# Performance work log

Hardware: AMD Instinct MI355X
Metric: run time of the kernel (lower is better)

## Reference

```python
import jax, jax.numpy as jnp
import numpy as np

N = 30000      # particles
E = 300000     # directed edges
H = 128        # hidden size
L = 10         # GNN layers
EMB = 16       # particle-type embedding size
T = 5          # velocity history window
NTYPES = 9
RADIUS = 0.05
OUT = 2
NODE_IN = 2 * T + 4 + EMB  # 30


def _mlp_ln(x, W1, b1, W2, b2, W3, b3, g, be):
    # Linear-ReLU-Linear-ReLU-Linear-LayerNorm (matches node/edge encoders and GraphNet blocks)
    h = jax.nn.relu(x @ W1 + b1)
    h = jax.nn.relu(h @ W2 + b2)
    h = h @ W3 + b3
    mu = jnp.mean(h, axis=-1, keepdims=True)
    var = jnp.mean((h - mu) ** 2, axis=-1, keepdims=True)
    return (h - mu) * jax.lax.rsqrt(var + 1e-5) * g + be


def setup_inputs() -> dict:
    key = jax.random.key(0)
    ks = iter(jax.random.split(key, 48))
    nx = lambda: next(ks)
    inp = {}
    inp["vel"] = jax.random.normal(nx(), (N, T, 2), jnp.float32) * 0.01
    inp["pos"] = jax.random.uniform(nx(), (N, 2), dtype=jnp.float32)
    inp["bounds"] = jnp.array([[0.0, 1.0], [0.0, 1.0]], jnp.float32)  # [dim, (lo,hi)]
    inp["tgt_pos"] = jax.random.uniform(nx(), (N, 2), dtype=jnp.float32)
    inp["particle_type"] = jax.random.randint(nx(), (N,), 0, NTYPES, jnp.int32)
    inp["nonk_mask"] = jax.random.randint(nx(), (N,), 0, 2, jnp.int32)
    inp["senders"] = jax.random.randint(nx(), (E,), 0, N, jnp.int32)
    inp["receivers"] = jax.random.randint(nx(), (E,), 0, N, jnp.int32)
    inp["emb"] = jax.random.normal(nx(), (NTYPES, EMB), jnp.float32) * 0.1

    def mlp_p(pre, din, lead=()):
        w = lambda i, o: jax.random.normal(nx(), lead + (i, o), jnp.float32) / np.sqrt(i)
        inp[pre + "_W1"] = w(din, H); inp[pre + "_b1"] = jnp.zeros(lead + (H,), jnp.float32)
        inp[pre + "_W2"] = w(H, H);   inp[pre + "_b2"] = jnp.zeros(lead + (H,), jnp.float32)
        inp[pre + "_W3"] = w(H, H);   inp[pre + "_b3"] = jnp.zeros(lead + (H,), jnp.float32)
        inp[pre + "_g"] = jnp.ones(lead + (H,), jnp.float32)
        inp[pre + "_be"] = jnp.zeros(lead + (H,), jnp.float32)

    mlp_p("ne", NODE_IN)          # node encoder
    mlp_p("ee", 3)                # edge encoder
    mlp_p("ge", 3 * H, (L,))      # per-layer edge-update MLPs
    mlp_p("gn", 2 * H, (L,))      # per-layer node-update MLPs
    inp["de_W1"] = jax.random.normal(nx(), (H, H), jnp.float32) / np.sqrt(H)
    inp["de_b1"] = jnp.zeros((H,), jnp.float32)
    inp["de_W2"] = jax.random.normal(nx(), (H, H), jnp.float32) / np.sqrt(H)
    inp["de_b2"] = jnp.zeros((H,), jnp.float32)
    inp["de_W3"] = jax.random.normal(nx(), (H, OUT), jnp.float32) / np.sqrt(H)
    inp["de_b3"] = jnp.zeros((OUT,), jnp.float32)
    return inp


def reference(vel, pos, bounds, tgt_pos, particle_type, nonk_mask, senders, receivers, emb,
              ne_W1, ne_b1, ne_W2, ne_b2, ne_W3, ne_b3, ne_g, ne_be,
              ee_W1, ee_b1, ee_W2, ee_b2, ee_W3, ee_b3, ee_g, ee_be,
              ge_W1, ge_b1, ge_W2, ge_b2, ge_W3, ge_b3, ge_g, ge_be,
              gn_W1, gn_b1, gn_W2, gn_b2, gn_W3, gn_b3, gn_g, gn_be,
              de_W1, de_b1, de_W2, de_b2, de_W3, de_b3):
    n = pos.shape[0]
    # --- construct node features ---
    vels = vel.reshape(n, -1)                                   # [N, T*2]
    dtw = jnp.concatenate([pos - bounds[:, 0], bounds[:, 1] - pos], axis=1)
    dtw = jnp.clip(dtw / RADIUS, -1.0, 1.0)                     # [N, 4]
    type_emb = emb[particle_type]                               # [N, EMB] gather
    node_attr = jnp.concatenate([vels, dtw, type_emb], axis=1)  # [N, 30]
    # --- construct edge features (senders/receivers precomputed; KD-tree is CPU-side) ---
    dist_vec = (pos[senders] - pos[receivers]) / RADIUS         # [E, 2]
    dist = jnp.linalg.norm(dist_vec, axis=1, keepdims=True)     # [E, 1]
    edge_attr = jnp.concatenate([dist_vec, dist], axis=1)       # [E, 3]
    # --- encode ---
    nodes = _mlp_ln(node_attr, ne_W1, ne_b1, ne_W2, ne_b2, ne_W3, ne_b3, ne_g, ne_be)
    edges = _mlp_ln(edge_attr, ee_W1, ee_b1, ee_W2, ee_b2, ee_W3, ee_b3, ee_g, ee_be)
    # --- process: L message-passing layers with residuals ---
    for l in range(ge_W1.shape[0]):
        e_in = jnp.concatenate([edges, nodes[senders], nodes[receivers]], axis=1)  # [E, 3H]
        edges = edges + _mlp_ln(e_in, ge_W1[l], ge_b1[l], ge_W2[l], ge_b2[l], ge_W3[l], ge_b3[l], ge_g[l], ge_be[l])
        agg = jax.ops.segment_sum(edges, receivers, num_segments=n)               # [N, H] scatter-add
        n_in = jnp.concatenate([nodes, agg], axis=1)                              # [N, 2H]
        nodes = nodes + _mlp_ln(n_in, gn_W1[l], gn_b1[l], gn_W2[l], gn_b2[l], gn_W3[l], gn_b3[l], gn_g[l], gn_be[l])
    # --- decode ---
    h = jax.nn.relu(nodes @ de_W1 + de_b1)
    h = jax.nn.relu(h @ de_W2 + de_b2)
    pred_acc = h @ de_W3 + de_b3                                 # [N, 2]
    # --- Euler integration step (out_size == 2 branch) ---
    pred_pos = pos + vel[:, -1, :] + pred_acc
    pred_pos = jnp.where(nonk_mask[:, None].astype(bool), pred_pos, tgt_pos)
    return pred_acc[:, None, :], pred_pos[:, None, :]
```

## Files before the change

### kernel.cpp

```cpp
#include <hip/hip_runtime.h>
#include <hip/hip_bf16.h>

typedef __hip_bfloat16 bf16;
typedef unsigned short u16;
typedef unsigned int u32;
typedef __attribute__((ext_vector_type(8))) short short8;
typedef __attribute__((ext_vector_type(4))) float f32x4;
typedef __attribute__((ext_vector_type(4))) unsigned int u32x4;

#define NPART 30000
#define NEDGE 300000
#define HD 128
#define NLAYER 10
#define NFLOAT_ARRAYS 43
#define NMAT 66

__device__ __forceinline__ bool detect_bf16(const unsigned short* braw) {
    return braw[1] == 0x3F80u;
}

__device__ __forceinline__ u16 f2b(float f) {
    const bf16 h = __float2bfloat16(f);
    u16 u;
    __builtin_memcpy(&u, &h, sizeof(u));
    return u;
}
__device__ __forceinline__ u32 pack2(float a, float b) {
    return (u32)f2b(a) | ((u32)f2b(b) << 16);
}
__device__ __forceinline__ float b2flo(u32 u) { return __uint_as_float(u << 16); }
__device__ __forceinline__ float b2fhi(u32 u) { return __uint_as_float(u & 0xFFFF0000u); }

__device__ __forceinline__ u32x4 ntl4(const u16* p) {
    return __builtin_nontemporal_load((const u32x4*)p);
}
__device__ __forceinline__ void nts4(const u32x4 v, u16* p) {
    __builtin_nontemporal_store(v, (u32x4*)p);
}
__device__ __forceinline__ f32x4 ntlf4(const float* p) {
    return __builtin_nontemporal_load((const f32x4*)p);
}
__device__ __forceinline__ void ntsf4(const f32x4 v, float* p) {
    __builtin_nontemporal_store(v, (f32x4*)p);
}

struct ConvArgs {
    const void* src[NFLOAT_ARRAYS];
    int n[NFLOAT_ARRAYS];
    int off[NFLOAT_ARRAYS];
};

__global__ __launch_bounds__(256)
void k_convert(ConvArgs a, float* __restrict__ dst, const unsigned short* __restrict__ braw)
{
    const bool isb = detect_bf16(braw);
    const int aid = blockIdx.y;
    const int n = a.n[aid];
    float* o = dst + a.off[aid];
    const int stride = gridDim.x * 256;
    int i = blockIdx.x * 256 + threadIdx.x;
    if (isb) {
        const unsigned short* s = (const unsigned short*)a.src[aid];
        for (; i < n; i += stride) {
            const unsigned int u = ((unsigned int)s[i]) << 16;
            o[i] = __uint_as_float(u);
        }
    } else {
        const float* s = (const float*)a.src[aid];
        for (; i < n; i += stride) o[i] = s[i];
    }
}

__global__ __launch_bounds__(256)
void k_hist(const int* __restrict__ rcv, int* __restrict__ counts)
{
    const int e = blockIdx.x * 256 + threadIdx.x;
    if (e < NEDGE) atomicAdd(&counts[rcv[e]], 1);
}

__global__ __launch_bounds__(1024)
void k_scan(const int* __restrict__ counts, int* __restrict__ row_ptr, int* __restrict__ cursor)
{
    __shared__ int part[1024];
    const int t = threadIdx.x;
    const int base = t * 32;
    int local[32];
    int s = 0;
#pragma unroll
    for (int k = 0; k < 32; k++) {
        const int idx = base + k;
        const int v = (idx < NPART) ? counts[idx] : 0;
        local[k] = s;
        s += v;
    }
    part[t] = s;
    __syncthreads();
    for (int off = 1; off < 1024; off <<= 1) {
        const int v = (t >= off) ? part[t - off] : 0;
        __syncthreads();
        part[t] += v;
        __syncthreads();
    }
    const int excl = (t == 0) ? 0 : part[t - 1];
#pragma unroll
    for (int k = 0; k < 32; k++) {
        const int idx = base + k;
        if (idx < NPART) {
            const int rp = excl + local[k];
            row_ptr[idx] = rp;
            cursor[idx] = rp;
        }
    }
    if (t == 0) row_ptr[NPART] = NEDGE;
}

__global__ __launch_bounds__(256)
void k_scatter(const int* __restrict__ snd, const int* __restrict__ rcv,
               int* __restrict__ cursor, int* __restrict__ snd_s, int* __restrict__ rcv_s)
{
    const int e = blockIdx.x * 256 + threadIdx.x;
    if (e < NEDGE) {
        const int r = rcv[e];
        const int p = atomicAdd(&cursor[r], 1);
        snd_s[p] = snd[e];
        rcv_s[p] = r;
    }
}

struct PackArgs {
    int src_off[NMAT];
    int dst_off[NMAT];
    int K[NMAT];
    int nks[NMAT];
};

__global__ __launch_bounds__(256)
void k_pack(const float* __restrict__ cw, u16* __restrict__ wpk, PackArgs pa)
{
    const int mid = blockIdx.y;
    const int nks = pa.nks[mid];
    const int total = nks * 4096;
    const int d = blockIdx.x * 256 + threadIdx.x;
    if (d >= total) return;
    const int j = d & 7, l = (d >> 3) & 63, t = d >> 9;
    const int ks = t % nks, mt = t / nks;
    const int hid = mt * 16 + (l & 15);
    const int k = ks * 32 + (l >> 4) * 8 + j;
    const float v = (k < pa.K[mid]) ? cw[pa.src_off[mid] + k * HD + hid] : 0.0f;
    wpk[pa.dst_off[mid] + d] = f2b(v);
}

template<int NKS, int XROW>
__device__ __forceinline__ void gemm16(const u16* __restrict__ Wp,
                                       const float* __restrict__ Bias,
                                       const u16* __restrict__ x,
                                       f32x4 acc[4][2],
                                       const int wm, const int wn,
                                       const int l15, const int lg, const int lane)
{
#pragma unroll
    for (int mt = 0; mt < 4; mt++) {
        const f32x4 bv = *(const f32x4*)(Bias + wm * 64 + mt * 16 + lg * 4);
        acc[mt][0] = bv;
        acc[mt][1] = bv;
    }
    const u16* xr0 = x + (wn * 32 + l15) * XROW + lg * 8;
    const u16* xr1 = xr0 + 16 * XROW;
    const u16* wp = Wp + (wm * 4 * NKS) * 512 + lane * 8;
#pragma unroll
    for (int ks = 0; ks < NKS; ks++) {
        const short8 b0 = *(const short8*)(xr0 + ks * 32);
        const short8 b1 = *(const short8*)(xr1 + ks * 32);
#pragma unroll
        for (int mt = 0; mt < 4; mt++) {
            const short8 a = *(const short8*)(wp + (mt * NKS + ks) * 512);
            acc[mt][0] = __builtin_amdgcn_mfma_f32_16x16x32_bf16(a, b0, acc[mt][0], 0, 0, 0);
            acc[mt][1] = __builtin_amdgcn_mfma_f32_16x16x32_bf16(a, b1, acc[mt][1], 0, 0, 0);
        }
    }
}

__device__ __forceinline__ void store_h(u16* __restrict__ h, const f32x4 acc[4][2],
                                        const int wm, const int wn, const int l15, const int lg)
{
#pragma unroll
    for (int nt = 0; nt < 2; nt++) {
        const int e = wn * 32 + nt * 16 + l15;
#pragma unroll
        for (int mt = 0; mt < 4; mt++) {
            const int hid = wm * 64 + mt * 16 + lg * 4;
            const f32x4 v = acc[mt][nt];
            const u32 lo = pack2(fmaxf(v[0], 0.0f), fmaxf(v[1], 0.0f));
            const u32 hi = pack2(fmaxf(v[2], 0.0f), fmaxf(v[3], 0.0f));
            *(uint2*)(h + e * 136 + hid) = make_uint2(lo, hi);
        }
    }
}

template<int NKS1, int XROW>
__device__ __forceinline__ void mlp_mfma(const u16* __restrict__ xs,
    u16* __restrict__ h1, u16* __restrict__ h2,
    float (*red)[2][2][16][2],
    const u16* __restrict__ W1p, const float* __restrict__ B1,
    const u16* __restrict__ W2p, const float* __restrict__ B2,
    const u16* __restrict__ W3p, const float* __restrict__ B3,
    const float* __restrict__ g, const float* __restrict__ be,
    float outv[4][2][4],
    const int wm, const int wn, const int l15, const int lg, const int lane)
{
    f32x4 acc[4][2];
    gemm16<NKS1, XROW>(W1p, B1, xs, acc, wm, wn, l15, lg, lane);
    __syncthreads();
    store_h(h1, acc, wm, wn, l15, lg);
    __syncthreads();
    gemm16<4, 136>(W2p, B2, h1, acc, wm, wn, l15, lg, lane);
    store_h(h2, acc, wm, wn, l15, lg);
    __syncthreads();
    gemm16<4, 136>(W3p, B3, h2, acc, wm, wn, l15, lg, lane);
    float ps[2], pss[2];
#pragma unroll
    for (int nt = 0; nt < 2; nt++) {
        float s = 0.0f, ss = 0.0f;
#pragma unroll
        for (int mt = 0; mt < 4; mt++) {
#pragma unroll
            for (int r = 0; r < 4; r++) {
                const float v = acc[mt][nt][r];
                s += v; ss += v * v;
            }
        }
        s += __shfl_xor(s, 16); ss += __shfl_xor(ss, 16);
        s += __shfl_xor(s, 32); ss += __shfl_xor(ss, 32);
        ps[nt] = s; pss[nt] = ss;
    }
    if (lane < 16) {
#pragma unroll
        for (int nt = 0; nt < 2; nt++) {
            red[wm][wn][nt][l15][0] = ps[nt];
            red[wm][wn][nt][l15][1] = pss[nt];
        }
    }
    __syncthreads();
#pragma unroll
    for (int nt = 0; nt < 2; nt++) {
        const float S  = red[0][wn][nt][l15][0] + red[1][wn][nt][l15][0];
        const float SS = red[0][wn][nt][l15][1] + red[1][wn][nt][l15][1];
        const float mu  = S * (1.0f / 128.0f);
        const float var = SS * (1.0f / 128.0f) - mu * mu;
        const float inv = rsqrtf(var + 1e-5f);
#pragma unroll
        for (int mt = 0; mt < 4; mt++) {
            const int hid = wm * 64 + mt * 16 + lg * 4;
            const f32x4 gv  = *(const f32x4*)(g + hid);
            const f32x4 bev = *(const f32x4*)(be + hid);
#pragma unroll
            for (int r = 0; r < 4; r++)
                outv[mt][nt][r] = (acc[mt][nt][r] - mu) * inv * gv[r] + bev[r];
        }
    }
}

__device__ __forceinline__ float nfeat(int i, int k,
    const float* __restrict__ vel, const float* __restrict__ pos,
    const float* __restrict__ bounds, const int* __restrict__ ptype,
    const float* __restrict__ emb)
{
    if (k < 10) return vel[i * 10 + k];
    if (k < 14) {
        const int q = k - 10;
        float sub;
        if (q < 2) sub = pos[i * 2 + q] - bounds[q * 2 + 0];
        else       sub = bounds[(q - 2) * 2 + 1] - pos[i * 2 + (q - 2)];
        const float dv = sub * 20.0f;
        return fminf(fmaxf(dv, -1.0f), 1.0f);
    }
    if (k < 30) return emb[ptype[i] * 16 + (k - 14)];
    return 0.0f;
}

__global__ __launch_bounds__(256)
void k_node_enc_m(const float* __restrict__ vel, const float* __restrict__ pos,
                  const float* __restrict__ bounds, const int* __restrict__ ptype,
                  const float* __restrict__ emb,
                  const u16* __restrict__ W1p, const float* __restrict__ B1,
                  const u16* __restrict__ W2p, const float* __restrict__ B2,
                  const u16* __restrict__ W3p, const float* __restrict__ B3,
                  const float* __restrict__ g, const float* __restrict__ be,
                  u16* __restrict__ nodes_bf)
{
    __shared__ __align__(16) u16 lds[17408];
    __shared__ float red[2][2][2][16][2];
    const int tid = threadIdx.x;
    const int i0 = blockIdx.x * 64;
    for (int idx = tid; idx < 1024; idx += 256) {
        const int m = idx >> 4, kk = idx & 15;
        const int i = i0 + m;
        float f0 = 0.0f, f1 = 0.0f;
        if (i < NPART) {
            f0 = nfeat(i, kk * 2 + 0, vel, pos, bounds, ptype, emb);
            f1 = nfeat(i, kk * 2 + 1, vel, pos, bounds, ptype, emb);
        }
        *(u32*)(lds + m * 40 + kk * 2) = pack2(f0, f1);
    }
    __syncthreads();
    const int lane = tid & 63, wv = tid >> 6;
    const int wm = wv >> 1, wn = wv & 1, l15 = lane & 15, lg = lane >> 4;
    float outv[4][2][4];
    mlp_mfma<1, 40>(lds, lds, lds + 8704, red, W1p, B1, W2p, B2, W3p, B3, g, be,
                    outv, wm, wn, l15, lg, lane);
#pragma unroll
    for (int nt = 0; nt < 2; nt++) {
        const int i = i0 + wn * 32 + nt * 16 + l15;
        if (i < NPART) {
#pragma unroll
            for (int mt = 0; mt < 4; mt++) {
                const int hid = wm * 64 + mt * 16 + lg * 4;
                *(uint2*)(nodes_bf + (size_t)i * HD + hid) =
                    make_uint2(pack2(outv[mt][nt][0], outv[mt][nt][1]),
                               pack2(outv[mt][nt][2], outv[mt][nt][3]));
            }
        }
    }
}

__global__ __launch_bounds__(256)
void k_edge_enc_m(const float* __restrict__ pos, const int* __restrict__ snd_s,
                  const int* __restrict__ rcv_s,
                  const u16* __restrict__ W1p, const float* __restrict__ B1,
                  const u16* __restrict__ W2p, const float* __restrict__ B2,
                  const u16* __restrict__ W3p, const float* __restrict__ B3,
                  const float* __restrict__ g, const float* __restrict__ be,
                  u16* __restrict__ edges_bf)
{
    __shared__ __align__(16) u16 lds[17408];
    __shared__ float red[2][2][2][16][2];
    const int tid = threadIdx.x;
    const int e0 = blockIdx.x * 64;
    for (int idx = tid; idx < 1024; idx += 256) {
        const int m = idx >> 4, kk = idx & 15;
        const int e = min(e0 + m, NEDGE - 1);
        u32 w = 0;
        if (kk < 2) {
            const int s = snd_s[e], r = rcv_s[e];
            const float dx = (pos[s * 2 + 0] - pos[r * 2 + 0]) * 20.0f;
            const float dy = (pos[s * 2 + 1] - pos[r * 2 + 1]) * 20.0f;
            if (kk == 0) w = pack2(dx, dy);
            else         w = pack2(sqrtf(dx * dx + dy * dy), 0.0f);
        }
        *(u32*)(lds + m * 40 + kk * 2) = w;
    }
    __syncthreads();
    const int lane = tid & 63, wv = tid >> 6;
    const int wm = wv >> 1, wn = wv & 1, l15 = lane & 15, lg = lane >> 4;
    float outv[4][2][4];
    mlp_mfma<1, 40>(lds, lds, lds + 8704, red, W1p, B1, W2p, B2, W3p, B3, g, be,
                    outv, wm, wn, l15, lg, lane);
#pragma unroll
    for (int nt = 0; nt < 2; nt++) {
        const int e = e0 + wn * 32 + nt * 16 + l15;
        if (e < NEDGE) {
#pragma unroll
            for (int mt = 0; mt < 4; mt++) {
                const int hid = wm * 64 + mt * 16 + lg * 4;
                *(uint2*)(edges_bf + (size_t)e * HD + hid) =
                    make_uint2(pack2(outv[mt][nt][0], outv[mt][nt][1]),
                               pack2(outv[mt][nt][2], outv[mt][nt][3]));
            }
        }
    }
}

__device__ __forceinline__ void egemm_seg32(const u16* __restrict__ Wp,
                                            const u16* __restrict__ x,
                                            f32x4 acc[2][2], const int ks0,
                                            const int wm,
                                            const int l15, const int lg, const int lane)
{
    const u16* xr0 = x + l15 * 136 + lg * 8;
    const u16* xr1 = xr0 + 16 * 136;
#pragma unroll
    for (int ks = 0; ks < 4; ks++) {
        const short8 b0 = *(const short8*)(xr0 + ks * 32);
        const short8 b1 = *(const short8*)(xr1 + ks * 32);
#pragma unroll
        for (int mt = 0; mt < 2; mt++) {
            const short8 a = *(const short8*)(Wp + (((wm * 2 + mt) * 12 + ks0 + ks) * 64 + lane) * 8);
            acc[mt][0] = __builtin_amdgcn_mfma_f32_16x16x32_bf16(a, b0, acc[mt][0], 0, 0, 0);
            acc[mt][1] = __builtin_amdgcn_mfma_f32_16x16x32_bf16(a, b1, acc[mt][1], 0, 0, 0);
        }
    }
}

__device__ __forceinline__ void egemm_h32(const u16* __restrict__ Wp,
                                          const float* __restrict__ Bias,
                                          const u16* __restrict__ x,
                                          f32x4 acc[2][2],
                                          const int wm,
                                          const int l15, const int lg, const int lane)
{
#pragma unroll
    for (int mt = 0; mt < 2; mt++) {
        const f32x4 bv = *(const f32x4*)(Bias + wm * 32 + mt * 16 + lg * 4);
        acc[mt][0] = bv;
        acc[mt][1] = bv;
    }
    const u16* xr0 = x + l15 * 136 + lg * 8;
    const u16* xr1 = xr0 + 16 * 136;
#pragma unroll
    for (int ks = 0; ks < 4; ks++) {
        const short8 b0 = *(const short8*)(xr0 + ks * 32);
        const short8 b1 = *(const short8*)(xr1 + ks * 32);
#pragma unroll
        for (int mt = 0; mt < 2; mt++) {
            const short8 a = *(const short8*)(Wp + (((wm * 2 + mt) * 4 + ks) * 64 + lane) * 8);
            acc[mt][0] = __builtin_amdgcn_mfma_f32_16x16x32_bf16(a, b0, acc[mt][0], 0, 0, 0);
            acc[mt][1] = __builtin_amdgcn_mfma_f32_16x16x32_bf16(a, b1, acc[mt][1], 0, 0, 0);
        }
    }
}

__device__ __forceinline__ void egemm_n1(const u16* __restrict__ Wp,
                                         const float* __restrict__ Bias,
                                         const u16* __restrict__ x,
                                         f32x4 acc[2][2],
                                         const int wm,
                                         const int l15, const int lg, const int lane)
{
#pragma unroll
    for (int mt = 0; mt < 2; mt++) {
        const f32x4 bv = *(const f32x4*)(Bias + wm * 32 + mt * 16 + lg * 4);
        acc[mt][0] = bv;
        acc[mt][1] = bv;
    }
    const u16* xr0 = x + l15 * 264 + lg * 8;
    const u16* xr1 = xr0 + 16 * 264;
#pragma unroll
    for (int ks = 0; ks < 8; ks++) {
        const short8 b0 = *(const short8*)(xr0 + ks * 32);
        const short8 b1 = *(const short8*)(xr1 + ks * 32);
#pragma unroll
        for (int mt = 0; mt < 2; mt++) {
            const short8 a = *(const short8*)(Wp + (((wm * 2 + mt) * 8 + ks) * 64 + lane) * 8);
            acc[mt][0] = __builtin_amdgcn_mfma_f32_16x16x32_bf16(a, b0, acc[mt][0], 0, 0, 0);
            acc[mt][1] = __builtin_amdgcn_mfma_f32_16x16x32_bf16(a, b1, acc[mt][1], 0, 0, 0);
        }
    }
}

__device__ __forceinline__ void estore_h32(u16* __restrict__ h, const f32x4 acc[2][2],
                                           const int wm, const int l15, const int lg)
{
#pragma unroll
    for (int nt = 0; nt < 2; nt++) {
        const int row = nt * 16 + l15;
#pragma unroll
        for (int mt = 0; mt < 2; mt++) {
            const int hid = wm * 32 + mt * 16 + lg * 4;
            const f32x4 v = acc[mt][nt];
            const u32 lo = pack2(fmaxf(v[0], 0.0f), fmaxf(v[1], 0.0f));
            const u32 hi = pack2(fmaxf(v[2], 0.0f), fmaxf(v[3], 0.0f));
            *(uint2*)(h + row * 136 + hid) = make_uint2(lo, hi);
        }
    }
}

__global__ __launch_bounds__(256, 8)
void k_edge_layer_m(const u16* __restrict__ nodes_bf, u16* __restrict__ edges_bf,
                    float* __restrict__ agg, float* __restrict__ bnd,
                    const int* __restrict__ snd_s, const int* __restrict__ rcv_s,
                    const u16* __restrict__ W1p, const float* __restrict__ B1,
                    const u16* __restrict__ W2p, const float* __restrict__ B2,
                    const u16* __restrict__ W3p, const float* __restrict__ B3,
                    const float* __restrict__ g, const float* __restrict__ be)
{
    __shared__ __align__(16) u16 sb[2 * 4352];
    __shared__ float red[4][2][16][2];
    __shared__ int rblk[34];
    u16* b0 = sb;
    u16* b1 = sb + 4352;
    float* fout = (float*)sb;

    const int tid = threadIdx.x;
    const int tile = blockIdx.x;
    const int e0 = tile * 32;
    const int lane = tid & 63, wm = tid >> 6;
    const int l15 = lane & 15, lg = lane >> 4;

    if (tid < 32)       rblk[tid] = rcv_s[e0 + tid];
    else if (tid == 32) rblk[32] = (e0 > 0) ? rcv_s[e0 - 1] : -2;
    else if (tid == 33) rblk[33] = (e0 + 32 < NEDGE) ? rcv_s[e0 + 32] : -2;

    u32x4 e_old[2];
#pragma unroll
    for (int t = 0; t < 2; t++) {
        const int idx = tid + t * 256;
        const int m = idx >> 4, q = idx & 15;
        e_old[t] = ntl4(edges_bf + (size_t)(e0 + m) * HD + q * 8);
        *(u32x4*)(b0 + m * 136 + q * 8) = e_old[t];
    }
    u32x4 st[2];
#pragma unroll
    for (int t = 0; t < 2; t++) {
        const int idx = tid + t * 256;
        const int m = idx >> 4, q = idx & 15;
        st[t] = *(const u32x4*)(nodes_bf + (size_t)snd_s[e0 + m] * HD + q * 8);
    }
    __syncthreads();

    f32x4 acc[2][2];
#pragma unroll
    for (int mt = 0; mt < 2; mt++) {
        const f32x4 bv = *(const f32x4*)(B1 + wm * 32 + mt * 16 + lg * 4);
        acc[mt][0] = bv;
        acc[mt][1] = bv;
    }
    __builtin_amdgcn_s_setprio(1);
    egemm_seg32(W1p, b0, acc, 0, wm, l15, lg, lane);
    __builtin_amdgcn_s_setprio(0);
#pragma unroll
    for (int t = 0; t < 2; t++) {
        const int idx = tid + t * 256;
        const int m = idx >> 4, q = idx & 15;
        *(u32x4*)(b1 + m * 136 + q * 8) = st[t];
    }
#pragma unroll
    for (int t = 0; t < 2; t++) {
        const int idx = tid + t * 256;
        const int m = idx >> 4, q = idx & 15;
        st[t] = *(const u32x4*)(nodes_bf + (size_t)rcv_s[e0 + m] * HD + q * 8);
    }
    __syncthreads();

    __builtin_amdgcn_s_setprio(1);
    egemm_seg32(W1p, b1, acc, 4, wm, l15, lg, lane);
    __builtin_amdgcn_s_setprio(0);
#pragma unroll
    for (int t = 0; t < 2; t++) {
        const int idx = tid + t * 256;
        const int m = idx >> 4, q = idx & 15;
        *(u32x4*)(b0 + m * 136 + q * 8) = st[t];
    }
    __syncthreads();

    __builtin_amdgcn_s_setprio(1);
    egemm_seg32(W1p, b0, acc, 8, wm, l15, lg, lane);
    __builtin_amdgcn_s_setprio(0);
    estore_h32(b1, acc, wm, l15, lg);
    __syncthreads();

    __builtin_amdgcn_s_setprio(1);
    egemm_h32(W2p, B2, b1, acc, wm, l15, lg, lane);
    __builtin_amdgcn_s_setprio(0);
    estore_h32(b0, acc, wm, l15, lg);
    __syncthreads();

    __builtin_amdgcn_s_setprio(1);
    egemm_h32(W3p, B3, b0, acc, wm, l15, lg, lane);
    __builtin_amdgcn_s_setprio(0);

    float ps[2], pss[2];
#pragma unroll
    for (int nt = 0; nt < 2; nt++) {
        float s = 0.0f, ss = 0.0f;
#pragma unroll
        for (int mt = 0; mt < 2; mt++) {
#pragma unroll
            for (int r = 0; r < 4; r++) {
                const float v = acc[mt][nt][r];
                s += v; ss += v * v;
            }
        }
        s += __shfl_xor(s, 16); ss += __shfl_xor(ss, 16);
        s += __shfl_xor(s, 32); ss += __shfl_xor(ss, 32);
        ps[nt] = s; pss[nt] = ss;
    }
    if (lane < 16) {
#pragma unroll
        for (int nt = 0; nt < 2; nt++) {
            red[wm][nt][l15][0] = ps[nt];
            red[wm][nt][l15][1] = pss[nt];
        }
    }
    __syncthreads();

#pragma unroll
    for (int nt = 0; nt < 2; nt++) {
        const float S  = red[0][nt][l15][0] + red[1][nt][l15][0]
                       + red[2][nt][l15][0] + red[3][nt][l15][0];
        const float SS = red[0][nt][l15][1] + red[1][nt][l15][1]
                       + red[2][nt][l15][1] + red[3][nt][l15][1];
        const float mu  = S * (1.0f / 128.0f);
        const float var = SS * (1.0f / 128.0f) - mu * mu;
        const float inv = rsqrtf(var + 1e-5f);
        const int row = nt * 16 + l15;
#pragma unroll
        for (int mt = 0; mt < 2; mt++) {
            const int hid = wm * 32 + mt * 16 + lg * 4;
            const f32x4 gv  = *(const f32x4*)(g + hid);
            const f32x4 bev = *(const f32x4*)(be + hid);
            f32x4 o;
#pragma unroll
            for (int r = 0; r < 4; r++)
                o[r] = (acc[mt][nt][r] - mu) * inv * gv[r] + bev[r];
            *(f32x4*)(fout + row * 132 + hid) = o;
        }
    }
    __syncthreads();

#pragma unroll
    for (int t = 0; t < 2; t++) {
        const int idx = tid + t * 256;
        const int m = idx >> 4, q = idx & 15;
        float4 lo = *(const float4*)(fout + m * 132 + q * 8);
        float4 hi = *(const float4*)(fout + m * 132 + q * 8 + 4);
        const u32x4 o = e_old[t];
        lo.x += b2flo(o.x); lo.y += b2fhi(o.x);
        lo.z += b2flo(o.y); lo.w += b2fhi(o.y);
        hi.x += b2flo(o.z); hi.y += b2fhi(o.z);
        hi.z += b2flo(o.w); hi.w += b2fhi(o.w);
        *(float4*)(fout + m * 132 + q * 8) = lo;
        *(float4*)(fout + m * 132 + q * 8 + 4) = hi;
        u32x4 nv;
        nv.x = pack2(lo.x, lo.y); nv.y = pack2(lo.z, lo.w);
        nv.z = pack2(hi.x, hi.y); nv.w = pack2(hi.z, hi.w);
        nts4(nv, edges_bf + (size_t)(e0 + m) * HD + q * 8);
    }
    __syncthreads();

    const int c = tid & 31;
    for (int ms = (tid >> 5); ms < 32; ms += 8) {
        const int rs = rblk[ms];
        if (ms > 0 && rblk[ms - 1] == rs) continue;
        int me = ms + 1;
        while (me < 32 && rblk[me] == rs) me++;
        f32x4 s = {0.0f, 0.0f, 0.0f, 0.0f};
        for (int m = ms; m < me; m++) {
            const float4 v = *(const float4*)(fout + m * 132 + c * 4);
            s.x += v.x; s.y += v.y; s.z += v.z; s.w += v.w;
        }
        const bool extb = (ms == 0 && rblk[32] == rs);
        const bool extf = (me == 32 && rblk[33] == rs);
        float* ap;
        if (!extb && !extf) ap = agg + (size_t)rs * HD + c * 4;
        else ap = bnd + ((size_t)tile * 2 + (extb ? 0 : 1)) * HD + c * 4;
        ntsf4(s, ap);
    }
}

__global__ __launch_bounds__(256)
void k_node_layer_m(u16* __restrict__ nodes_bf,
                    const float* __restrict__ agg, const float* __restrict__ bnd,
                    const int* __restrict__ row_ptr,
                    const u16* __restrict__ W1p, const float* __restrict__ B1,
                    const u16* __restrict__ W2p, const float* __restrict__ B2,
                    const u16* __restrict__ W3p, const float* __restrict__ B3,
                    const float* __restrict__ g, const float* __restrict__ be)
{
    __shared__ __align__(16) u16 xs[32 * 264];
    __shared__ __align__(16) u16 hb[32 * 136];
    __shared__ float red[4][2][16][2];
    __shared__ int rp[33];
    const int tid = threadIdx.x;
    const int i0 = blockIdx.x * 32;
    const int lane = tid & 63, wm = tid >> 6;
    const int l15 = lane & 15, lg = lane >> 4;
    if (tid < 33) rp[tid] = row_ptr[min(i0 + tid, NPART)];
    __syncthreads();
#pragma unroll
    for (int t = 0; t < 2; t++) {
        const int idx = tid + t * 256;
        const int m = idx >> 4, q = idx & 15;
        const int i = min(i0 + m, NPART - 1);
        *(u32x4*)(xs + m * 264 + q * 8) =
            *(const u32x4*)(nodes_bf + (size_t)i * HD + q * 8);
    }
#pragma unroll
    for (int t = 0; t < 2; t++) {
        const int idx = tid + t * 256;
        const int m = idx >> 4, q = idx & 15;
        const int i = i0 + m;
        f32x4 a = {0.0f, 0.0f, 0.0f, 0.0f};
        f32x4 b = {0.0f, 0.0f, 0.0f, 0.0f};
        if (i < NPART) {
            const int p0 = rp[m], p1 = rp[m + 1];
            if (p1 > p0) {
                const int b0i = p0 >> 5, b1i = (p1 - 1) >> 5;
                if (b0i == b1i) {
                    const float* src = agg + (size_t)i * HD + q * 8;
                    a = ntlf4(src);
                    b = ntlf4(src + 4);
                } else {
                    const float* s1 = bnd + ((size_t)b0i * 2 + 1) * HD + q * 8;
                    a = ntlf4(s1);
                    b = ntlf4(s1 + 4);
                    for (int bb = b0i + 1; bb <= b1i; bb++) {
                        const float* s0 = bnd + ((size_t)bb * 2 + 0) * HD + q * 8;
                        a += ntlf4(s0);
                        b += ntlf4(s0 + 4);
                    }
                }
            }
        }
        *(u32x4*)(xs + m * 264 + 128 + q * 8) = (u32x4){
            pack2(a.x, a.y), pack2(a.z, a.w), pack2(b.x, b.y), pack2(b.z, b.w)};
    }
    __syncthreads();

    f32x4 acc[2][2];
    __builtin_amdgcn_s_setprio(1);
    egemm_n1(W1p, B1, xs, acc, wm, l15, lg, lane);
    __builtin_amdgcn_s_setprio(0);
    estore_h32(hb, acc, wm, l15, lg);
    __syncthreads();
    __builtin_amdgcn_s_setprio(1);
    egemm_h32(W2p, B2, hb, acc, wm, l15, lg, lane);
    __builtin_amdgcn_s_setprio(0);
    estore_h32(xs, acc, wm, l15, lg);
    __syncthreads();
    __builtin_amdgcn_s_setprio(1);
    egemm_h32(W3p, B3, xs, acc, wm, l15, lg, lane);
    __builtin_amdgcn_s_setprio(0);

    float ps[2], pss[2];
#pragma unroll
    for (int nt = 0; nt < 2; nt++) {
        float s = 0.0f, ss = 0.0f;
#pragma unroll
        for (int mt = 0; mt < 2; mt++) {
#pragma unroll
            for (int r = 0; r < 4; r++) {
                const float v = acc[mt][nt][r];
                s += v; ss += v * v;
            }
        }
        s += __shfl_xor(s, 16); ss += __shfl_xor(ss, 16);
        s += __shfl_xor(s, 32); ss += __shfl_xor(ss, 32);
        ps[nt] = s; pss[nt] = ss;
    }
    if (lane < 16) {
#pragma unroll
        for (int nt = 0; nt < 2; nt++) {
            red[wm][nt][l15][0] = ps[nt];
            red[wm][nt][l15][1] = pss[nt];
        }
    }
    __syncthreads();

#pragma unroll
    for (int nt = 0; nt < 2; nt++) {
        const float S  = red[0][nt][l15][0] + red[1][nt][l15][0]
                       + red[2][nt][l15][0] + red[3][nt][l15][0];
        const float SS = red[0][nt][l15][1] + red[1][nt][l15][1]
                       + red[2][nt][l15][1] + red[3][nt][l15][1];
        const float mu  = S * (1.0f / 128.0f);
        const float var = SS * (1.0f / 128.0f) - mu * mu;
        const float inv = rsqrtf(var + 1e-5f);
        const int i = i0 + nt * 16 + l15;
        if (i < NPART) {
            u16* np = nodes_bf + (size_t)i * HD;
#pragma unroll
            for (int mt = 0; mt < 2; mt++) {
                const int hid = wm * 32 + mt * 16 + lg * 4;
                const f32x4 gv  = *(const f32x4*)(g + hid);
                const f32x4 bev = *(const f32x4*)(be + hid);
                const uint2 ob = *(const uint2*)(np + hid);
                float4 nv;
                nv.x = b2flo(ob.x) + (acc[mt][nt][0] - mu) * inv * gv[0] + bev[0];
                nv.y = b2fhi(ob.x) + (acc[mt][nt][1] - mu) * inv * gv[1] + bev[1];
                nv.z = b2flo(ob.y) + (acc[mt][nt][2] - mu) * inv * gv[2] + bev[2];
                nv.w = b2fhi(ob.y) + (acc[mt][nt][3] - mu) * inv * gv[3] + bev[3];
                *(uint2*)(np + hid) = make_uint2(pack2(nv.x, nv.y), pack2(nv.z, nv.w));
            }
        }
    }
}

template<int K, int S>
__device__ __forceinline__ void gemv(const float* __restrict__ in,
                                     const float* __restrict__ W,
                                     const float* __restrict__ B,
                                     float acc[8])
{
    const int j = threadIdx.x;
    const float bb = B[j];
#pragma unroll
    for (int m = 0; m < 8; m++) acc[m] = bb;
    constexpr int K4 = (K / 4) * 4;
    for (int k = 0; k < K4; k += 4) {
        const float w0 = W[(k + 0) * HD + j];
        const float w1 = W[(k + 1) * HD + j];
        const float w2 = W[(k + 2) * HD + j];
        const float w3 = W[(k + 3) * HD + j];
#pragma unroll
        for (int m = 0; m < 8; m++) {
            const float4 x = *(const float4*)(in + m * S + k);
            float a = acc[m];
            a = fmaf(x.x, w0, a);
            a = fmaf(x.y, w1, a);
            a = fmaf(x.z, w2, a);
            a = fmaf(x.w, w3, a);
            acc[m] = a;
        }
    }
#pragma unroll
    for (int k = K4; k < K; k++) {
        const float w = W[k * HD + j];
#pragma unroll
        for (int m = 0; m < 8; m++) acc[m] = fmaf(in[m * S + k], w, acc[m]);
    }
}

__global__ __launch_bounds__(128)
void k_decoder(const u16* __restrict__ nodes_bf,
               const float* W1, const float* B1, const float* W2, const float* B2,
               const float* W3, const float* B3,
               const float* __restrict__ vel, const float* __restrict__ pos,
               const float* __restrict__ tgt, const int* __restrict__ nonk,
               const unsigned short* __restrict__ braw, void* __restrict__ d_out)
{
    __shared__ __align__(16) float xs[8 * HD];
    __shared__ __align__(16) float h1[8 * HD];
    __shared__ __align__(16) float h2[8 * HD];
    const int j = threadIdx.x;
    const int i0 = blockIdx.x * 8;
    float acc[8];
    for (int idx = j; idx < 512; idx += 128) {
        const int m = idx >> 6, q = idx & 63;
        const u32 w = *(const u32*)(nodes_bf + (size_t)(i0 + m) * HD + q * 2);
        xs[m * HD + q * 2]     = b2flo(w);
        xs[m * HD + q * 2 + 1] = b2fhi(w);
    }
    __syncthreads();
    gemv<HD, HD>(xs, W1, B1, acc);
#pragma unroll
    for (int m = 0; m < 8; m++) h1[m * HD + j] = fmaxf(acc[m], 0.0f);
    __syncthreads();
    gemv<HD, HD>(h1, W2, B2, acc);
#pragma unroll
    for (int m = 0; m < 8; m++) h2[m * HD + j] = fmaxf(acc[m], 0.0f);
    __syncthreads();
    if (j < 16) {
        const int m = j >> 1, d = j & 1, i = i0 + m;
        float a = B3[d];
        for (int k = 0; k < HD; k++) a = fmaf(h2[m * HD + k], W3[k * 2 + d], a);
        float pp = pos[i * 2 + d] + vel[i * 10 + 8 + d] + a;
        if (nonk[i] == 0) pp = tgt[i * 2 + d];
        if (detect_bf16(braw)) {
            bf16* o = (bf16*)d_out;
            o[i * 2 + d] = __float2bfloat16(a);
            o[2 * NPART + i * 2 + d] = __float2bfloat16(pp);
        } else {
            float* o = (float*)d_out;
            o[i * 2 + d] = a;
            o[2 * NPART + i * 2 + d] = pp;
        }
    }
}

extern "C" void kernel_launch(void* const* d_in, const int* in_sizes, int n_in,
                              void* d_out, int out_size, void* d_ws, size_t ws_size,
                              hipStream_t stream)
{
    const int* ptype = (const int*)d_in[4];
    const int* nonk  = (const int*)d_in[5];
    const int* snd   = (const int*)d_in[6];
    const int* rcv   = (const int*)d_in[7];
    const unsigned short* braw = (const unsigned short*)d_in[2];

    int fmap[NFLOAT_ARRAYS];
    {
        int c = 0;
        fmap[c++] = 0; fmap[c++] = 1; fmap[c++] = 2; fmap[c++] = 3; fmap[c++] = 8;
        for (int i = 9; i <= 46; i++) fmap[c++] = i;
    }
    ConvArgs ca;
    const float* fp[47];
    float* cw = (float*)d_ws;
    int off = 0;
    for (int i = 0; i < NFLOAT_ARRAYS; i++) {
        ca.src[i] = d_in[fmap[i]];
        ca.n[i]   = in_sizes[fmap[i]];
        ca.off[i] = off;
        fp[fmap[i]] = cw + off;
        off += in_sizes[fmap[i]];
    }
    const int EB32 = NEDGE / 32;
    float* agg   = cw + ((off + 3) & ~3);
    float* bnd   = agg + (size_t)NPART * HD;
    u16* edges_bf = (u16*)(bnd + (size_t)EB32 * 2 * HD);
    u16* nodes_bf = edges_bf + (size_t)NEDGE * HD;
    u16* wpk = nodes_bf + (size_t)NPART * HD;

    PackArgs pa;
    int dst = 0, c = 0;
    int pk[NMAT];
    auto addm = [&](long srcoff, int K) {
        const int nk = (K + 31) / 32;
        pa.src_off[c] = (int)srcoff;
        pa.K[c] = K;
        pa.nks[c] = nk;
        pa.dst_off[c] = dst;
        pk[c] = dst;
        dst += nk * 4096;
        c++;
    };
    addm(fp[9]  - cw, 30);  addm(fp[11] - cw, 128); addm(fp[13] - cw, 128);
    addm(fp[17] - cw, 3);   addm(fp[19] - cw, 128); addm(fp[21] - cw, 128);
    for (int l = 0; l < NLAYER; l++) {
        addm(fp[25] - cw + (long)l * 384 * HD, 384);
        addm(fp[27] - cw + (long)l * HD * HD, 128);
        addm(fp[29] - cw + (long)l * HD * HD, 128);
    }
    for (int l = 0; l < NLAYER; l++) {
        addm(fp[33] - cw + (long)l * 256 * HD, 256);
        addm(fp[35] - cw + (long)l * HD * HD, 128);
        addm(fp[37] - cw + (long)l * HD * HD, 128);
    }

    int* ip = (int*)(wpk + ((dst + 7) & ~7));
    int* row_ptr = ip;            ip += NPART + 8;
    int* cursor  = ip;            ip += NPART;
    int* counts  = ip;            ip += NPART;
    int* snd_s   = ip;            ip += NEDGE;
    int* rcv_s   = ip;

    const int EBL = (NEDGE + 255) / 256;

    k_convert<<<dim3(64, NFLOAT_ARRAYS), 256, 0, stream>>>(ca, cw, braw);
    hipMemsetAsync(counts, 0, (size_t)NPART * sizeof(int), stream);
    k_hist<<<EBL, 256, 0, stream>>>(rcv, counts);
    k_scan<<<1, 1024, 0, stream>>>(counts, row_ptr, cursor);
    k_scatter<<<EBL, 256, 0, stream>>>(snd, rcv, cursor, snd_s, rcv_s);
    k_pack<<<dim3(192, NMAT), 256, 0, stream>>>(cw, wpk, pa);

    const int NB = (NPART + 63) / 64;
    const int NB32 = (NPART + 31) / 32;
    const int EB = (NEDGE + 63) / 64;

    k_node_enc_m<<<NB, 256, 0, stream>>>(fp[0], fp[1], fp[2], ptype, fp[8],
        wpk + pk[0], fp[10], wpk + pk[1], fp[12], wpk + pk[2], fp[14],
        fp[15], fp[16], nodes_bf);
    k_edge_enc_m<<<EB, 256, 0, stream>>>(fp[1], snd_s, rcv_s,
        wpk + pk[3], fp[18], wpk + pk[4], fp[20], wpk + pk[5], fp[22],
        fp[23], fp[24], edges_bf);

    for (int l = 0; l < NLAYER; l++) {
        k_edge_layer_m<<<EB32, 256, 0, stream>>>(nodes_bf, edges_bf, agg, bnd, snd_s, rcv_s,
            wpk + pk[6 + 3 * l],  fp[26] + (size_t)l * HD,
            wpk + pk[7 + 3 * l],  fp[28] + (size_t)l * HD,
            wpk + pk[8 + 3 * l],  fp[30] + (size_t)l * HD,
            fp[31] + (size_t)l * HD, fp[32] + (size_t)l * HD);
        k_node_layer_m<<<NB32, 256, 0, stream>>>(nodes_bf, agg, bnd, row_ptr,
            wpk + pk[36 + 3 * l], fp[34] + (size_t)l * HD,
            wpk + pk[37 + 3 * l], fp[36] + (size_t)l * HD,
            wpk + pk[38 + 3 * l], fp[38] + (size_t)l * HD,
            fp[39] + (size_t)l * HD, fp[40] + (size_t)l * HD);
    }

    k_decoder<<<NPART / 8, 128, 0, stream>>>(nodes_bf,
        fp[41], fp[42], fp[43], fp[44], fp[45], fp[46],
        fp[0], fp[1], fp[3], nonk, braw, d_out);
}
```

Measured before the change: 1.893 ms.

## Store aggregation buffers in bf16 and dedupe receiver-node gathers per tile

```diff
diff --git a/kernel.cpp b/kernel.cpp
--- a/kernel.cpp
+++ b/kernel.cpp
@@ -7,6 +7,7 @@
 typedef __attribute__((ext_vector_type(8))) short short8;
 typedef __attribute__((ext_vector_type(4))) float f32x4;
 typedef __attribute__((ext_vector_type(4))) unsigned int u32x4;
+typedef __attribute__((ext_vector_type(2))) unsigned int u32x2;
 
 #define NPART 30000
 #define NEDGE 300000
@@ -37,11 +38,8 @@
 __device__ __forceinline__ void nts4(const u32x4 v, u16* p) {
     __builtin_nontemporal_store(v, (u32x4*)p);
 }
-__device__ __forceinline__ f32x4 ntlf4(const float* p) {
-    return __builtin_nontemporal_load((const f32x4*)p);
-}
-__device__ __forceinline__ void ntsf4(const f32x4 v, float* p) {
-    __builtin_nontemporal_store(v, (f32x4*)p);
+__device__ __forceinline__ void ntu2(const u32x2 v, u16* p) {
+    __builtin_nontemporal_store(v, (u32x2*)p);
 }
 
 struct ConvArgs {
@@ -391,6 +389,27 @@
     }
 }
 
+__device__ __forceinline__ void egemm_seg32_r(const u16* __restrict__ Wp,
+                                              const u16* __restrict__ x,
+                                              f32x4 acc[2][2], const int ks0,
+                                              const int wm, const int r0, const int r1,
+                                              const int lg, const int lane)
+{
+    const u16* xr0 = x + r0 * 136 + lg * 8;
+    const u16* xr1 = x + r1 * 136 + lg * 8;
+#pragma unroll
+    for (int ks = 0; ks < 4; ks++) {
+        const short8 b0 = *(const short8*)(xr0 + ks * 32);
+        const short8 b1 = *(const short8*)(xr1 + ks * 32);
+#pragma unroll
+        for (int mt = 0; mt < 2; mt++) {
+            const short8 a = *(const short8*)(Wp + (((wm * 2 + mt) * 12 + ks0 + ks) * 64 + lane) * 8);
+            acc[mt][0] = __builtin_amdgcn_mfma_f32_16x16x32_bf16(a, b0, acc[mt][0], 0, 0, 0);
+            acc[mt][1] = __builtin_amdgcn_mfma_f32_16x16x32_bf16(a, b1, acc[mt][1], 0, 0, 0);
+        }
+    }
+}
+
 __device__ __forceinline__ void egemm_h32(const u16* __restrict__ Wp,
                                           const float* __restrict__ Bias,
                                           const u16* __restrict__ x,
@@ -466,7 +485,7 @@
 
 __global__ __launch_bounds__(256, 8)
 void k_edge_layer_m(const u16* __restrict__ nodes_bf, u16* __restrict__ edges_bf,
-                    float* __restrict__ agg, float* __restrict__ bnd,
+                    u16* __restrict__ agg_bf, u16* __restrict__ bnd_bf,
                     const int* __restrict__ snd_s, const int* __restrict__ rcv_s,
                     const u16* __restrict__ W1p, const float* __restrict__ B1,
                     const u16* __restrict__ W2p, const float* __restrict__ B2,
@@ -476,6 +495,7 @@
     __shared__ __align__(16) u16 sb[2 * 4352];
     __shared__ float red[4][2][16][2];
     __shared__ int rblk[34];
+    __shared__ int srow[32];
     u16* b0 = sb;
     u16* b1 = sb + 4352;
     float* fout = (float*)sb;
@@ -507,6 +527,13 @@
     }
     __syncthreads();
 
+    if (tid < 32) {
+        const int r = rblk[tid];
+        int j = tid;
+        while (j > 0 && rblk[j - 1] == r) j--;
+        srow[tid] = j;
+    }
+
     f32x4 acc[2][2];
 #pragma unroll
     for (int mt = 0; mt < 2; mt++) {
@@ -527,7 +554,9 @@
     for (int t = 0; t < 2; t++) {
         const int idx = tid + t * 256;
         const int m = idx >> 4, q = idx & 15;
-        st[t] = *(const u32x4*)(nodes_bf + (size_t)rcv_s[e0 + m] * HD + q * 8);
+        const bool is_start = (m == 0) || (rblk[m] != rblk[m - 1]);
+        if (is_start)
+            st[t] = *(const u32x4*)(nodes_bf + (size_t)rblk[m] * HD + q * 8);
     }
     __syncthreads();
 
@@ -538,12 +567,15 @@
     for (int t = 0; t < 2; t++) {
         const int idx = tid + t * 256;
         const int m = idx >> 4, q = idx & 15;
-        *(u32x4*)(b0 + m * 136 + q * 8) = st[t];
-    }
-    __syncthreads();
-
+        const bool is_start = (m == 0) || (rblk[m] != rblk[m - 1]);
+        if (is_start)
+            *(u32x4*)(b0 + m * 136 + q * 8) = st[t];
+    }
+    __syncthreads();
+
+    const int sr0 = srow[l15], sr1 = srow[16 + l15];
     __builtin_amdgcn_s_setprio(1);
-    egemm_seg32(W1p, b0, acc, 8, wm, l15, lg, lane);
+    egemm_seg32_r(W1p, b0, acc, 8, wm, sr0, sr1, lg, lane);
     __builtin_amdgcn_s_setprio(0);
     estore_h32(b1, acc, wm, l15, lg);
     __syncthreads();
@@ -638,18 +670,19 @@
             const float4 v = *(const float4*)(fout + m * 132 + c * 4);
             s.x += v.x; s.y += v.y; s.z += v.z; s.w += v.w;
         }
+        const u32x2 pv = {pack2(s.x, s.y), pack2(s.z, s.w)};
         const bool extb = (ms == 0 && rblk[32] == rs);
         const bool extf = (me == 32 && rblk[33] == rs);
-        float* ap;
-        if (!extb && !extf) ap = agg + (size_t)rs * HD + c * 4;
-        else ap = bnd + ((size_t)tile * 2 + (extb ? 0 : 1)) * HD + c * 4;
-        ntsf4(s, ap);
+        u16* ap;
+        if (!extb && !extf) ap = agg_bf + (size_t)rs * HD + c * 4;
+        else ap = bnd_bf + ((size_t)tile * 2 + (extb ? 0 : 1)) * HD + c * 4;
+        ntu2(pv, ap);
     }
 }
 
 __global__ __launch_bounds__(256)
 void k_node_layer_m(u16* __restrict__ nodes_bf,
-                    const float* __restrict__ agg, const float* __restrict__ bnd,
+                    const u16* __restrict__ agg_bf, const u16* __restrict__ bnd_bf,
                     const int* __restrict__ row_ptr,
                     const u16* __restrict__ W1p, const float* __restrict__ B1,
                     const u16* __restrict__ W2p, const float* __restrict__ B2,
@@ -679,30 +712,28 @@
         const int idx = tid + t * 256;
         const int m = idx >> 4, q = idx & 15;
         const int i = i0 + m;
-        f32x4 a = {0.0f, 0.0f, 0.0f, 0.0f};
-        f32x4 b = {0.0f, 0.0f, 0.0f, 0.0f};
+        u32x4 w = {0u, 0u, 0u, 0u};
         if (i < NPART) {
             const int p0 = rp[m], p1 = rp[m + 1];
             if (p1 > p0) {
                 const int b0i = p0 >> 5, b1i = (p1 - 1) >> 5;
                 if (b0i == b1i) {
-                    const float* src = agg + (size_t)i * HD + q * 8;
-                    a = ntlf4(src);
-                    b = ntlf4(src + 4);
+                    w = ntl4(agg_bf + (size_t)i * HD + q * 8);
                 } else {
-                    const float* s1 = bnd + ((size_t)b0i * 2 + 1) * HD + q * 8;
-                    a = ntlf4(s1);
-                    b = ntlf4(s1 + 4);
+                    u32x4 p = ntl4(bnd_bf + ((size_t)b0i * 2 + 1) * HD + q * 8);
+                    f32x4 a = {b2flo(p.x), b2fhi(p.x), b2flo(p.y), b2fhi(p.y)};
+                    f32x4 b = {b2flo(p.z), b2fhi(p.z), b2flo(p.w), b2fhi(p.w)};
                     for (int bb = b0i + 1; bb <= b1i; bb++) {
-                        const float* s0 = bnd + ((size_t)bb * 2 + 0) * HD + q * 8;
-                        a += ntlf4(s0);
-                        b += ntlf4(s0 + 4);
+                        p = ntl4(bnd_bf + ((size_t)bb * 2 + 0) * HD + q * 8);
+                        a += (f32x4){b2flo(p.x), b2fhi(p.x), b2flo(p.y), b2fhi(p.y)};
+                        b += (f32x4){b2flo(p.z), b2fhi(p.z), b2flo(p.w), b2fhi(p.w)};
                     }
+                    w = (u32x4){pack2(a[0], a[1]), pack2(a[2], a[3]),
+                                pack2(b[0], b[1]), pack2(b[2], b[3])};
                 }
             }
         }
-        *(u32x4*)(xs + m * 264 + 128 + q * 8) = (u32x4){
-            pack2(a.x, a.y), pack2(a.z, a.w), pack2(b.x, b.y), pack2(b.z, b.w)};
+        *(u32x4*)(xs + m * 264 + 128 + q * 8) = w;
     }
     __syncthreads();
 
@@ -885,11 +916,11 @@
         off += in_sizes[fmap[i]];
     }
     const int EB32 = NEDGE / 32;
-    float* agg   = cw + ((off + 3) & ~3);
-    float* bnd   = agg + (size_t)NPART * HD;
-    u16* edges_bf = (u16*)(bnd + (size_t)EB32 * 2 * HD);
+    u16* edges_bf = (u16*)(cw + ((off + 3) & ~3));
     u16* nodes_bf = edges_bf + (size_t)NEDGE * HD;
-    u16* wpk = nodes_bf + (size_t)NPART * HD;
+    u16* agg_bf   = nodes_bf + (size_t)NPART * HD;
+    u16* bnd_bf   = agg_bf + (size_t)NPART * HD;
+    u16* wpk      = bnd_bf + (size_t)EB32 * 2 * HD;
 
     PackArgs pa;
     int dst = 0, c = 0;
@@ -945,12 +976,13 @@
         fp[23], fp[24], edges_bf);
 
     for (int l = 0; l < NLAYER; l++) {
-        k_edge_layer_m<<<EB32, 256, 0, stream>>>(nodes_bf, edges_bf, agg, bnd, snd_s, rcv_s,
+        k_edge_layer_m<<<EB32, 256, 0, stream>>>(nodes_bf, edges_bf, agg_bf, bnd_bf,
+            snd_s, rcv_s,
             wpk + pk[6 + 3 * l],  fp[26] + (size_t)l * HD,
             wpk + pk[7 + 3 * l],  fp[28] + (size_t)l * HD,
             wpk + pk[8 + 3 * l],  fp[30] + (size_t)l * HD,
             fp[31] + (size_t)l * HD, fp[32] + (size_t)l * HD);
-        k_node_layer_m<<<NB32, 256, 0, stream>>>(nodes_bf, agg, bnd, row_ptr,
+        k_node_layer_m<<<NB32, 256, 0, stream>>>(nodes_bf, agg_bf, bnd_bf, row_ptr,
             wpk + pk[36 + 3 * l], fp[34] + (size_t)l * HD,
             wpk + pk[37 + 3 * l], fp[36] + (size_t)l * HD,
             wpk + pk[38 + 3 * l], fp[38] + (size_t)l * HD,
```

After: 1.807 ms (median of 2 runs). 4.5% less time.
